# Kernel optimization log

Measured on AMD Instinct MI355X. Metric: run time of the kernel, lower is better.

The kernel has to match this reference:

```python
import jax, jax.numpy as jnp
import numpy as np

B, S, W = 16, 512, 5
H, E, V = 512, 256, 100000


def setup_inputs() -> dict:
    key = jax.random.key(0)
    ks = jax.random.split(key, 20)
    inp = {
        "hiddens": jax.random.normal(ks[0], (B, S, H), jnp.float32),
        "masks": jax.random.randint(ks[1], (B, S), 0, 2, jnp.int32),
        "begins": jax.random.randint(ks[2], (B, S, W), 0, V, jnp.int32),
        "begin_lens": jax.random.randint(ks[3], (B, S), 0, W + 1, jnp.int32),
        "middles": jax.random.randint(ks[4], (B, S, W), 0, V, jnp.int32),
        "middle_lens": jax.random.randint(ks[5], (B, S), 0, W + 1, jnp.int32),
        "ends": jax.random.randint(ks[6], (B, S, W), 0, V, jnp.int32),
        "end_lens": jax.random.randint(ks[7], (B, S), 0, W + 1, jnp.int32),
        # parameters
        "emb": jax.random.normal(ks[8], (V, E), jnp.float32) * 0.02,
        "W_hidden": jax.random.normal(ks[9], (H, 3 * H), jnp.float32) * (1.0 / np.sqrt(H)),
        "b_hidden": jnp.zeros((3 * H,), jnp.float32),
        "W_begin": jax.random.normal(ks[10], (E, 2 * H), jnp.float32) * (1.0 / np.sqrt(E)),
        "b_begin": jnp.zeros((2 * H,), jnp.float32),
        "W_middle": jax.random.normal(ks[11], (E, 2 * H), jnp.float32) * (1.0 / np.sqrt(E)),
        "b_middle": jnp.zeros((2 * H,), jnp.float32),
        "W_end": jax.random.normal(ks[12], (E, 2 * H), jnp.float32) * (1.0 / np.sqrt(E)),
        "b_end": jnp.zeros((2 * H,), jnp.float32),
        "W_gate": jax.random.normal(ks[13], (H, 9), jnp.float32) * (1.0 / np.sqrt(H)),
        "b_gate": jnp.zeros((9,), jnp.float32),
    }
    return inp


def _len_mask(lens, w):
    # True where the lattice candidate is valid (mimics _make_mask's 1s)
    return jnp.arange(w)[None, None, :] < lens[:, :, None]


def _gates(hiddens, masks, W_gate, b_gate):
    b, s, _ = hiddens.shape
    lmr = hiddens @ W_gate + b_gate                      # (B,S,9)
    left, mid, right = jnp.split(lmr, 3, axis=-1)        # each (B,S,3)
    g = jax.nn.sigmoid(left[:, :-2] + mid[:, 1:-1] + right[:, 2:])  # (B,S-2,3)
    ones = jnp.ones((b, 1), g.dtype)
    zeros = jnp.zeros((b, 1), g.dtype)
    begin_g = jnp.concatenate([ones, g[..., 0], ones], axis=1)
    mid_g = jnp.concatenate([zeros, g[..., 1], zeros], axis=1)
    end_g = jnp.concatenate([ones, g[..., 2], ones], axis=1)
    pad = masks == 0
    z = jnp.zeros((), g.dtype)
    return (jnp.where(pad, z, begin_g), jnp.where(pad, z, mid_g), jnp.where(pad, z, end_g))


def reference(hiddens, masks, begins, begin_lens, middles, middle_lens, ends, end_lens,
              emb, W_hidden, b_hidden, W_begin, b_begin, W_middle, b_middle,
              W_end, b_end, W_gate, b_gate):
    w = begins.shape[-1]
    begin_m = _len_mask(begin_lens, w)
    middle_m = _len_mask(middle_lens, w)
    end_m = _len_mask(end_lens, w)

    begin_kv = emb[begins] @ W_begin + b_begin           # (B,S,W,2H)
    middle_kv = emb[middles] @ W_middle + b_middle
    end_kv = emb[ends] @ W_end + b_end

    query, hidden_key, hidden_value = jnp.split(hiddens @ W_hidden + b_hidden, 3, axis=-1)
    bg, mg, eg = _gates(hiddens, masks, W_gate, b_gate)
    begin_kv = bg[:, :, None, None] * begin_kv
    middle_kv = mg[:, :, None, None] * middle_kv
    end_kv = eg[:, :, None, None] * end_kv

    kv = jnp.concatenate([begin_kv, middle_kv, end_kv], axis=-2)   # (B,S,3W,2H)
    h = hiddens.shape[-1]
    keys, values = jnp.split(kv, 2, axis=-1)
    keys = jnp.concatenate([hidden_key[:, :, None, :], keys], axis=-2)     # (B,S,1+3W,H)
    values = jnp.concatenate([hidden_value[:, :, None, :], values], axis=-2)

    # combined mask: True entries get -1e10 (faithful to masked_fill_(masks, -1e10))
    score_mask = jnp.concatenate(
        [(masks != 0)[:, :, None], begin_m, middle_m, end_m], axis=-1)     # (B,S,1+3W)

    scores = jnp.einsum("bsh,bskh->bsk", query, keys)
    scores = jnp.where(score_mask, jnp.asarray(-1e10, scores.dtype), scores)
    weights = jax.nn.softmax(scores, axis=-1)
    return jnp.einsum("bsk,bskh->bsh", weights, values)
```

## Files before the change

kernel.cpp:

```cpp
#include <hip/hip_runtime.h>
#include <cstdint>
#include <cstddef>


typedef unsigned short u16;
typedef _Float16 f16;
typedef __attribute__((ext_vector_type(8))) f16 f16x8;
typedef __attribute__((ext_vector_type(4))) float f32x4;

#define MROWS 8192
#define SS 512

static __device__ __forceinline__ u16 f2h(float x) {
  f16 h = (f16)x;
  return __builtin_bit_cast(u16, h);
}
static __device__ __forceinline__ float h2f(u16 h) {
  return (float)__builtin_bit_cast(f16, h);
}
static __device__ __forceinline__ float sigm(float x) { return 1.f / (1.f + __expf(-x)); }

static __device__ __forceinline__ void gl2lds(const u16* g, u16* l) {
  __builtin_amdgcn_global_load_lds(
      (const __attribute__((address_space(1))) unsigned int*)g,
      (__attribute__((address_space(3))) unsigned int*)l, 16, 0, 0);
}

__global__ __launch_bounds__(256) void prep_xlmr(
    const float* __restrict__ X, const float* __restrict__ Wg,
    const float* __restrict__ bg, u16* __restrict__ Xh,
    float* __restrict__ lmr, float* __restrict__ s0) {
  __shared__ float wg[4608];
  const int t = threadIdx.x;
  if (blockIdx.x < 32) s0[blockIdx.x * 256 + t] = 0.f;
  for (int i = t; i < 4608; i += 256) wg[i] = Wg[i];
  __syncthreads();
  const int lane = t & 63, wid = t >> 6;
#pragma unroll
  for (int it = 0; it < 4; it++) {
    int pos = blockIdx.x * 16 + it * 4 + wid;
    const float* x = X + (size_t)pos * 512 + lane * 8;
    float4 x0 = *(const float4*)x;
    float4 x1 = *(const float4*)(x + 4);
    float xs[8] = {x0.x, x0.y, x0.z, x0.w, x1.x, x1.y, x1.z, x1.w};
    ushort4 h0, h1;
    h0.x = f2h(xs[0]); h0.y = f2h(xs[1]); h0.z = f2h(xs[2]); h0.w = f2h(xs[3]);
    h1.x = f2h(xs[4]); h1.y = f2h(xs[5]); h1.z = f2h(xs[6]); h1.w = f2h(xs[7]);
    ((ushort4*)Xh)[pos * 128 + lane * 2] = h0;
    ((ushort4*)Xh)[pos * 128 + lane * 2 + 1] = h1;
    float p[9];
#pragma unroll
    for (int c = 0; c < 9; c++) p[c] = 0.f;
    const float* wrow = wg + (lane * 8) * 9;
#pragma unroll
    for (int j = 0; j < 8; j++)
#pragma unroll
      for (int c = 0; c < 9; c++) p[c] += xs[j] * wrow[j * 9 + c];
#pragma unroll
    for (int c = 0; c < 9; c++)
#pragma unroll
      for (int o = 32; o > 0; o >>= 1) p[c] += __shfl_xor(p[c], o);
    if (lane == 0) {
#pragma unroll
      for (int c = 0; c < 9; c++) lmr[(size_t)pos * 9 + c] = p[c] + bg[c];
    }
  }
}

__global__ __launch_bounds__(256) void prep_weights(
    const float* __restrict__ Wh, const float* __restrict__ Wb,
    const float* __restrict__ Wm, const float* __restrict__ We,
    const float* __restrict__ bb, const float* __restrict__ bm,
    const float* __restrict__ be, const float* __restrict__ bh,
    const float* __restrict__ lmr, const int* __restrict__ masks,
    u16* __restrict__ Breg, u16* __restrict__ Acat, u16* __restrict__ Whq,
    u16* __restrict__ WvT, float* __restrict__ gates, float* __restrict__ bcat,
    float* __restrict__ u, float* __restrict__ cbuf) {
  __shared__ float tile[64][65];
  const int b = blockIdx.x;
  const int t = threadIdx.x;
  if (b < 64) {
    int k0 = (b & 7) * 64;
    int n0 = (b >> 3) * 64;
#pragma unroll
    for (int i = 0; i < 16; i++) {
      int li = i * 256 + t; int r = li >> 6, c = li & 63;
      tile[r][c] = Wh[(size_t)(k0 + r) * 1536 + 1024 + n0 + c];
    }
    __syncthreads();
#pragma unroll
    for (int i = 0; i < 16; i++) {
      int li = i * 256 + t; int r = li >> 6, c = li & 63;
      Breg[(size_t)(512 + n0 + r) * 512 + k0 + c] = f2h(tile[c][r]);
    }
  } else if (b < 128) {
#pragma unroll
    for (int i = 0; i < 4; i++) {
      int q4 = (b - 64) * 1024 + t * 4 + i;
      int k = q4 >> 7;
      int c4 = (q4 & 127) * 4;
      float4 vq = *(const float4*)(Wh + (size_t)k * 1536 + c4);
      float4 vk = *(const float4*)(Wh + (size_t)k * 1536 + 512 + c4);
      ushort4 qh, kh;
      qh.x = f2h(vq.x); qh.y = f2h(vq.y); qh.z = f2h(vq.z); qh.w = f2h(vq.w);
      kh.x = f2h(vk.x); kh.y = f2h(vk.y); kh.z = f2h(vk.z); kh.w = f2h(vk.w);
      size_t o = (size_t)k * 512 + c4;
      *(ushort4*)(Whq + o) = qh;
      *(ushort4*)(Acat + o) = kh;
    }
  } else if (b < 576) {
    int tid = (b - 128) * 256 + t;
    int n = tid >> 7;
    int kq = (tid & 127) * 4;
    float4 v;
    if (n < 768) {
      int ty = n >> 8, c = n & 255;
      const float* src = (ty == 0 ? Wb : ty == 1 ? Wm : We) + (size_t)c * 1024 + kq;
      v = *(const float4*)src;
    } else if (n < 771) {
      int ty = n - 768;
      const float* src = (ty == 0 ? bb : ty == 1 ? bm : be) + kq;
      v = *(const float4*)src;
    } else {
      v = make_float4(0.f, 0.f, 0.f, 0.f);
    }
    ushort4 h; h.x = f2h(v.x); h.y = f2h(v.y); h.z = f2h(v.z); h.w = f2h(v.w);
    ((ushort4*)(Acat + (size_t)512 * 512))[tid] = h;
  } else if (b < 672) {
    int idx = b - 576;
    int ty = idx >> 5;
    int rem = idx & 31;
    int c0 = (rem & 3) * 64;
    int n0 = (rem >> 2) * 64;
    const float* Wsrc = ty == 0 ? Wb : ty == 1 ? Wm : We;
#pragma unroll
    for (int i = 0; i < 16; i++) {
      int li = i * 256 + t; int r = li >> 6, c = li & 63;
      tile[r][c] = Wsrc[(size_t)(c0 + r) * 1024 + 512 + n0 + c];
    }
    __syncthreads();
#pragma unroll
    for (int i = 0; i < 16; i++) {
      int li = i * 256 + t; int r = li >> 6, c = li & 63;
      WvT[(size_t)(n0 + r) * 768 + ty * 256 + c0 + c] = f2h(tile[c][r]);
    }
  } else if (b < 704) {
    int pos = (b - 672) * 256 + t;
    int s = pos & (SS - 1);
    float g0, g1, g2;
    if (masks[pos] == 0) {
      g0 = g1 = g2 = 0.f;
    } else if (s == 0 || s == SS - 1) {
      g0 = 1.f; g1 = 0.f; g2 = 1.f;
    } else {
      const float* p0 = lmr + (size_t)(pos - 1) * 9;
      const float* p1 = lmr + (size_t)pos * 9;
      const float* p2 = lmr + (size_t)(pos + 1) * 9;
      g0 = sigm(p0[0] + p1[3] + p2[6]);
      g1 = sigm(p0[1] + p1[4] + p2[7]);
      g2 = sigm(p0[2] + p1[5] + p2[8]);
    }
    gates[(size_t)pos * 3 + 0] = g0;
    gates[(size_t)pos * 3 + 1] = g1;
    gates[(size_t)pos * 3 + 2] = g2;
  } else {
    const int lane = t & 63;
    const int widx = (b - 704) * 4 + (t >> 6);
    const int c = lane * 8;
    if (widx < 896) {
      int n = widx;
      float acc = 0.f;
      if (n < 768) {
        int ty = n >> 8, ce = n & 255;
        const float* src = (ty == 0 ? Wb : ty == 1 ? Wm : We) + (size_t)ce * 1024 + c;
        float4 a0 = *(const float4*)src;
        float4 a1 = *(const float4*)(src + 4);
        float4 b0 = *(const float4*)(bh + c);
        float4 b1 = *(const float4*)(bh + c + 4);
        acc = a0.x * b0.x + a0.y * b0.y + a0.z * b0.z + a0.w * b0.w +
              a1.x * b1.x + a1.y * b1.y + a1.z * b1.z + a1.w * b1.w;
      } else if (n < 771) {
        int ty = n - 768;
        const float* src = (ty == 0 ? bb : ty == 1 ? bm : be) + c;
        float4 a0 = *(const float4*)src;
        float4 a1 = *(const float4*)(src + 4);
        float4 b0 = *(const float4*)(bh + c);
        float4 b1 = *(const float4*)(bh + c + 4);
        acc = a0.x * b0.x + a0.y * b0.y + a0.z * b0.z + a0.w * b0.w +
              a1.x * b1.x + a1.y * b1.y + a1.z * b1.z + a1.w * b1.w;
      }
#pragma unroll
      for (int o = 32; o > 0; o >>= 1) acc += __shfl_xor(acc, o);
      if (lane == 0) bcat[512 + n] = acc;
    } else if (widx < 1408) {
      int k = widx - 896;
      const float* wr = Wh + (size_t)k * 1536;
      float4 a0 = *(const float4*)(wr + c);
      float4 a1 = *(const float4*)(wr + c + 4);
      float4 a2 = *(const float4*)(wr + 512 + c);
      float4 a3 = *(const float4*)(wr + 512 + c + 4);
      float4 b0 = *(const float4*)(bh + 512 + c);
      float4 b1 = *(const float4*)(bh + 512 + c + 4);
      float4 b2 = *(const float4*)(bh + c);
      float4 b3 = *(const float4*)(bh + c + 4);
      float acc = a0.x * b0.x + a0.y * b0.y + a0.z * b0.z + a0.w * b0.w +
                  a1.x * b1.x + a1.y * b1.y + a1.z * b1.z + a1.w * b1.w +
                  a2.x * b2.x + a2.y * b2.y + a2.z * b2.z + a2.w * b2.w +
                  a3.x * b3.x + a3.y * b3.y + a3.z * b3.z + a3.w * b3.w;
#pragma unroll
      for (int o = 32; o > 0; o >>= 1) acc += __shfl_xor(acc, o);
      if (lane == 0) u[k] = acc;
    } else if (widx == 1408) {
      float4 b0 = *(const float4*)(bh + c);
      float4 b1 = *(const float4*)(bh + c + 4);
      float4 b2 = *(const float4*)(bh + 512 + c);
      float4 b3 = *(const float4*)(bh + 512 + c + 4);
      float acc = b0.x * b2.x + b0.y * b2.y + b0.z * b2.z + b0.w * b2.w +
                  b1.x * b3.x + b1.y * b3.y + b1.z * b3.z + b1.w * b3.w;
#pragma unroll
      for (int o = 32; o > 0; o >>= 1) acc += __shfl_xor(acc, o);
      if (lane == 0) cbuf[0] = acc;
    } else if (widx < 1417) {
      int i = (widx - 1409) * 64 + lane;
      bcat[i] = bh[1024 + i];
    }
  }
}

template <int MODE>
__global__ __launch_bounds__(256) void gemm_k(
    const u16* __restrict__ A, const u16* __restrict__ Bt,
    const float* __restrict__ ubias, const float* __restrict__ bcat,
    float* __restrict__ Cf, u16* __restrict__ Cb, int Kdim,
    const float* __restrict__ Xf, float* __restrict__ s0) {
  __shared__ __align__(16) u16 As[128 * 32];
  __shared__ __align__(16) u16 Bs[128 * 32];

  const int t = threadIdx.x;
  const int lane = t & 63;
  const int wid = t >> 6;
  const int m0 = blockIdx.x * 128;
  const int n0 = blockIdx.y * 128;
  const int wm = (wid & 1) * 64;
  const int wn = (wid >> 1) * 64;
  const int fr = lane & 15;
  const int kq = (lane >> 4) * 8;

  f32x4 acc[4][4];
#pragma unroll
  for (int i = 0; i < 4; i++)
#pragma unroll
    for (int j = 0; j < 4; j++) acc[i][j] = (f32x4){0.f, 0.f, 0.f, 0.f};

  for (int k0 = 0; k0 < Kdim; k0 += 32) {
    __syncthreads();
#pragma unroll
    for (int p = 0; p < 2; p++) {
      int li = p * 256 + t;
      int row = li >> 2;
      int so = (li & 3) * 8;
      gl2lds(&A[(size_t)(m0 + row) * Kdim + k0 + so], &As[li * 8]);
      gl2lds(&Bt[(size_t)(n0 + row) * Kdim + k0 + so], &Bs[li * 8]);
    }
    __syncthreads();
    f16x8 av[4], bv[4];
#pragma unroll
    for (int i = 0; i < 4; i++) {
      av[i] = *(const f16x8*)&As[(wm + i * 16 + fr) * 32 + kq];
      bv[i] = *(const f16x8*)&Bs[(wn + i * 16 + fr) * 32 + kq];
    }
#pragma unroll
    for (int mt = 0; mt < 4; mt++)
#pragma unroll
      for (int nt = 0; nt < 4; nt++)
        acc[mt][nt] = __builtin_amdgcn_mfma_f32_16x16x32_f16(
            av[mt], bv[nt], acc[mt][nt], 0, 0, 0);
  }

  const int r0 = (lane >> 4) * 4;
  if constexpr (MODE == 0) {
    if (blockIdx.y < 4) {
      float pl[4][4];
#pragma unroll
      for (int mt = 0; mt < 4; mt++)
#pragma unroll
        for (int r = 0; r < 4; r++) pl[mt][r] = 0.f;
#pragma unroll
      for (int mt = 0; mt < 4; mt++)
#pragma unroll
        for (int nt = 0; nt < 4; nt++) {
          int col = n0 + wn + nt * 16 + fr;
          float bv2 = ubias[col];
#pragma unroll
          for (int r = 0; r < 4; r++) {
            int row = m0 + wm + mt * 16 + r0 + r;
            pl[mt][r] += (acc[mt][nt][r] + bv2) * Xf[(size_t)row * 512 + col];
          }
        }
#pragma unroll
      for (int mt = 0; mt < 4; mt++)
#pragma unroll
        for (int r = 0; r < 4; r++) {
          float p = pl[mt][r];
          p += __shfl_xor(p, 1);
          p += __shfl_xor(p, 2);
          p += __shfl_xor(p, 4);
          p += __shfl_xor(p, 8);
          if (fr == r) {
            int row = m0 + wm + mt * 16 + r0 + r;
            atomicAdd(&s0[row], p);
          }
        }
      return;
    }
#pragma unroll
    for (int mt = 0; mt < 4; mt++)
#pragma unroll
      for (int nt = 0; nt < 4; nt++) {
        int col = n0 - 512 + wn + nt * 16 + fr;
        float bv2 = bcat[col];
#pragma unroll
        for (int r = 0; r < 4; r++) {
          int row = m0 + wm + mt * 16 + r0 + r;
          float v = acc[mt][nt][r] + bv2;
          if (col < 512) Cf[(size_t)row * 512 + col] = v;
          else Cb[(size_t)row * 896 + (col - 512)] = f2h(v);
        }
      }
  } else if constexpr (MODE == 1) {
#pragma unroll
    for (int mt = 0; mt < 4; mt++)
#pragma unroll
      for (int nt = 0; nt < 4; nt++) {
        int col = n0 + wn + nt * 16 + fr;
#pragma unroll
        for (int r = 0; r < 4; r++) {
          int row = m0 + wm + mt * 16 + r0 + r;
          int orow = row < 512 ? row : row + 512;
          Cb[(size_t)orow * 512 + col] = f2h(acc[mt][nt][r]);
        }
      }
  } else {
#pragma unroll
    for (int mt = 0; mt < 4; mt++)
#pragma unroll
      for (int nt = 0; nt < 4; nt++) {
        int col = n0 + wn + nt * 16 + fr;
#pragma unroll
        for (int r = 0; r < 4; r++) {
          int row = m0 + wm + mt * 16 + r0 + r;
          Cf[(size_t)row * 512 + col] += acc[mt][nt][r];
        }
      }
  }
}

__global__ __launch_bounds__(256) void attn_kernel(
    const int* __restrict__ masks, const int* __restrict__ begins,
    const int* __restrict__ blens, const int* __restrict__ middles,
    const int* __restrict__ mlens, const int* __restrict__ ends,
    const int* __restrict__ elens, const float* __restrict__ emb,
    const float* __restrict__ HV, const u16* __restrict__ Pb,
    const float* __restrict__ gates, const float* __restrict__ b_begin,
    const float* __restrict__ b_middle, const float* __restrict__ b_end,
    const float* __restrict__ s0buf, const float* __restrict__ cbuf,
    float* __restrict__ out, u16* __restrict__ Ebar) {
  __shared__ float bvs[3][512];
  {
    int tt = threadIdx.x;
    for (int i = tt; i < 512; i += 256) {
      bvs[0][i] = b_begin[512 + i];
      bvs[1][i] = b_middle[512 + i];
      bvs[2][i] = b_end[512 + i];
    }
  }
  __syncthreads();
  const int t = threadIdx.x;
  const int lane = t & 63;
  const int wid = t >> 6;
  const int pos = blockIdx.x * 4 + wid;
  const int mask = masks[pos];
  const float* hvp = HV + (size_t)pos * 512;
  float4 hv0 = *(const float4*)(hvp + lane * 8);
  float4 hv1 = *(const float4*)(hvp + lane * 8 + 4);
  float* orow = out + (size_t)pos * 512;
  u16* erow = Ebar + (size_t)pos * 768;

  if (mask == 0) {
    float s0 = s0buf[pos] + cbuf[0];
    int nv = min(blens[pos], 5) + min(mlens[pos], 5) + min(elens[pos], 5);
    int ninv = 15 - nv;
    float w0;
    if (ninv == 0) {
      w0 = 1.f;
    } else {
      float Mx = fmaxf(s0, 0.f);
      float e0 = __expf(s0 - Mx);
      w0 = e0 / (e0 + (float)ninv * __expf(-Mx));
    }
    float4 o0, o1;
    o0.x = w0 * hv0.x; o0.y = w0 * hv0.y; o0.z = w0 * hv0.z; o0.w = w0 * hv0.w;
    o1.x = w0 * hv1.x; o1.y = w0 * hv1.y; o1.z = w0 * hv1.z; o1.w = w0 * hv1.w;
    *(float4*)(orow + lane * 8) = o0;
    *(float4*)(orow + lane * 8 + 4) = o1;
    ushort4 zz; zz.x = zz.y = zz.z = zz.w = 0;
    *(ushort4*)(erow + 0 * 256 + lane * 4) = zz;
    *(ushort4*)(erow + 1 * 256 + lane * 4) = zz;
    *(ushort4*)(erow + 2 * 256 + lane * 4) = zz;
  } else {
    float g[3];
    g[0] = gates[(size_t)pos * 3 + 0];
    g[1] = gates[(size_t)pos * 3 + 1];
    g[2] = gates[(size_t)pos * 3 + 2];
    const u16* prow = Pb + (size_t)pos * 896;
    float4 Pt[3];
    float qb[3];
#pragma unroll
    for (int ty = 0; ty < 3; ty++) {
      ushort4 pu = *(const ushort4*)(prow + ty * 256 + lane * 4);
      Pt[ty].x = h2f(pu.x); Pt[ty].y = h2f(pu.y);
      Pt[ty].z = h2f(pu.z); Pt[ty].w = h2f(pu.w);
      qb[ty] = h2f(prow[768 + ty]);
    }
    int lens[3] = {blens[pos], mlens[pos], elens[pos]};
    const int* ib = begins + (size_t)pos * 5;
    const int* im = middles + (size_t)pos * 5;
    const int* ie = ends + (size_t)pos * 5;
    float4 ev[3][5];
#pragma unroll
    for (int w = 0; w < 5; w++) {
      ev[0][w] = *(const float4*)(emb + (size_t)ib[w] * 256 + lane * 4);
      ev[1][w] = *(const float4*)(emb + (size_t)im[w] * 256 + lane * 4);
      ev[2][w] = *(const float4*)(emb + (size_t)ie[w] * 256 + lane * 4);
    }
    float sc[16];
    sc[0] = -1e10f;
#pragma unroll
    for (int ty = 0; ty < 3; ty++) {
#pragma unroll
      for (int w = 0; w < 5; w++) {
        float4 e = ev[ty][w];
        float d = Pt[ty].x * e.x + Pt[ty].y * e.y + Pt[ty].z * e.z + Pt[ty].w * e.w;
#pragma unroll
        for (int o = 32; o > 0; o >>= 1) d += __shfl_xor(d, o);
        sc[1 + ty * 5 + w] = (w < lens[ty]) ? -1e10f : g[ty] * (d + qb[ty]);
      }
    }
    float Mx = sc[0];
#pragma unroll
    for (int k = 1; k < 16; k++) Mx = fmaxf(Mx, sc[k]);
    float wts[16];
    float zs = 0.f;
#pragma unroll
    for (int k = 0; k < 16; k++) {
      wts[k] = __expf(sc[k] - Mx);
      zs += wts[k];
    }
    float inv = 1.f / zs;
    float alpha[3];
#pragma unroll
    for (int ty = 0; ty < 3; ty++) {
      float ax = 0.f, ay = 0.f, az = 0.f, aw = 0.f, asum = 0.f;
#pragma unroll
      for (int w = 0; w < 5; w++) {
        float wk = wts[1 + ty * 5 + w];
        asum += wk;
        ax += wk * ev[ty][w].x;
        ay += wk * ev[ty][w].y;
        az += wk * ev[ty][w].z;
        aw += wk * ev[ty][w].w;
      }
      float sg = g[ty] * inv;
      alpha[ty] = sg * asum;
      ushort4 h;
      h.x = f2h(ax * sg); h.y = f2h(ay * sg); h.z = f2h(az * sg); h.w = f2h(aw * sg);
      *(ushort4*)(erow + ty * 256 + lane * 4) = h;
    }
    float w0 = wts[0] * inv;
    float4 o0, o1;
    int hb = lane * 8;
    o0.x = w0 * hv0.x + alpha[0] * bvs[0][hb + 0] + alpha[1] * bvs[1][hb + 0] + alpha[2] * bvs[2][hb + 0];
    o0.y = w0 * hv0.y + alpha[0] * bvs[0][hb + 1] + alpha[1] * bvs[1][hb + 1] + alpha[2] * bvs[2][hb + 1];
    o0.z = w0 * hv0.z + alpha[0] * bvs[0][hb + 2] + alpha[1] * bvs[1][hb + 2] + alpha[2] * bvs[2][hb + 2];
    o0.w = w0 * hv0.w + alpha[0] * bvs[0][hb + 3] + alpha[1] * bvs[1][hb + 3] + alpha[2] * bvs[2][hb + 3];
    o1.x = w0 * hv1.x + alpha[0] * bvs[0][hb + 4] + alpha[1] * bvs[1][hb + 4] + alpha[2] * bvs[2][hb + 4];
    o1.y = w0 * hv1.y + alpha[0] * bvs[0][hb + 5] + alpha[1] * bvs[1][hb + 5] + alpha[2] * bvs[2][hb + 5];
    o1.z = w0 * hv1.z + alpha[0] * bvs[0][hb + 6] + alpha[1] * bvs[1][hb + 6] + alpha[2] * bvs[2][hb + 6];
    o1.w = w0 * hv1.w + alpha[0] * bvs[0][hb + 7] + alpha[1] * bvs[1][hb + 7] + alpha[2] * bvs[2][hb + 7];
    *(float4*)(orow + lane * 8) = o0;
    *(float4*)(orow + lane * 8 + 4) = o1;
  }
}

extern "C" void kernel_launch(void* const* d_in, const int* in_sizes, int n_in,
                              void* d_out, int out_size, void* d_ws, size_t ws_size,
                              hipStream_t stream) {
  const float* hiddens = (const float*)d_in[0];
  const int* masks = (const int*)d_in[1];
  const int* begins = (const int*)d_in[2];
  const int* blens = (const int*)d_in[3];
  const int* middles = (const int*)d_in[4];
  const int* mlens = (const int*)d_in[5];
  const int* ends = (const int*)d_in[6];
  const int* elens = (const int*)d_in[7];
  const float* emb = (const float*)d_in[8];
  const float* Wh = (const float*)d_in[9];
  const float* bh = (const float*)d_in[10];
  const float* Wb = (const float*)d_in[11];
  const float* bb = (const float*)d_in[12];
  const float* Wm = (const float*)d_in[13];
  const float* bm = (const float*)d_in[14];
  const float* We = (const float*)d_in[15];
  const float* be = (const float*)d_in[16];
  const float* Wg = (const float*)d_in[17];
  const float* bg = (const float*)d_in[18];
  float* out = (float*)d_out;

  char* ws = (char*)d_ws;
  size_t off = 0;
  auto alloc = [&](size_t bytes) -> char* {
    char* p = ws + off;
    off += (bytes + 255) & ~(size_t)255;
    return p;
  };
  u16* Xh = (u16*)alloc((size_t)8192 * 512 * 2);
  u16* Whq = (u16*)alloc((size_t)512 * 512 * 2);
  u16* Acat = (u16*)alloc((size_t)1408 * 512 * 2);
  u16* Breg = (u16*)alloc((size_t)1920 * 512 * 2);
  u16* WvT = (u16*)alloc((size_t)512 * 768 * 2);
  float* HV = (float*)alloc((size_t)8192 * 512 * 4);
  u16* Pb = (u16*)alloc((size_t)8192 * 896 * 2);
  float* lmr = (float*)alloc((size_t)8192 * 9 * 4);
  float* gates = (float*)alloc((size_t)8192 * 3 * 4);
  float* s0 = (float*)alloc((size_t)8192 * 4);
  float* bcat = (float*)alloc((size_t)1408 * 4);
  float* u = (float*)alloc((size_t)512 * 4);
  float* cbuf = (float*)alloc((size_t)4);
  u16* Ebar = (u16*)alloc((size_t)8192 * 768 * 2);
  if (off > ws_size) return;

  prep_xlmr<<<512, 256, 0, stream>>>(hiddens, Wg, bg, Xh, lmr, s0);
  prep_weights<<<1059, 256, 0, stream>>>(Wh, Wb, Wm, We, bb, bm, be, bh, lmr,
                                         masks, Breg, Acat, Whq, WvT, gates,
                                         bcat, u, cbuf);
  gemm_k<1><<<dim3(11, 4), 256, 0, stream>>>(
      Acat, Whq, nullptr, nullptr, nullptr, Breg, 512, nullptr, nullptr);
  gemm_k<0><<<dim3(64, 15), 256, 0, stream>>>(
      Xh, Breg, u, bcat, HV, Pb, 512, hiddens, s0);
  attn_kernel<<<2048, 256, 0, stream>>>(masks, begins, blens, middles, mlens, ends,
                                        elens, emb, HV, Pb, gates, bb, bm, be,
                                        s0, cbuf, out, Ebar);
  gemm_k<2><<<dim3(64, 4), 256, 0, stream>>>(
      Ebar, WvT, nullptr, nullptr, out, nullptr, 768, nullptr, nullptr);
}
```

Measured before the change: 290.2 us.

## Merge prep kernels, store hidden values in fp16, fold output combine into final GEMM

```diff
diff --git a/kernel.cpp b/kernel.cpp
--- a/kernel.cpp
+++ b/kernel.cpp
@@ -26,57 +26,18 @@
       (__attribute__((address_space(3))) unsigned int*)l, 16, 0, 0);
 }
 
-__global__ __launch_bounds__(256) void prep_xlmr(
+__global__ __launch_bounds__(256) void prep_all(
     const float* __restrict__ X, const float* __restrict__ Wg,
-    const float* __restrict__ bg, u16* __restrict__ Xh,
-    float* __restrict__ lmr, float* __restrict__ s0) {
-  __shared__ float wg[4608];
-  const int t = threadIdx.x;
-  if (blockIdx.x < 32) s0[blockIdx.x * 256 + t] = 0.f;
-  for (int i = t; i < 4608; i += 256) wg[i] = Wg[i];
-  __syncthreads();
-  const int lane = t & 63, wid = t >> 6;
-#pragma unroll
-  for (int it = 0; it < 4; it++) {
-    int pos = blockIdx.x * 16 + it * 4 + wid;
-    const float* x = X + (size_t)pos * 512 + lane * 8;
-    float4 x0 = *(const float4*)x;
-    float4 x1 = *(const float4*)(x + 4);
-    float xs[8] = {x0.x, x0.y, x0.z, x0.w, x1.x, x1.y, x1.z, x1.w};
-    ushort4 h0, h1;
-    h0.x = f2h(xs[0]); h0.y = f2h(xs[1]); h0.z = f2h(xs[2]); h0.w = f2h(xs[3]);
-    h1.x = f2h(xs[4]); h1.y = f2h(xs[5]); h1.z = f2h(xs[6]); h1.w = f2h(xs[7]);
-    ((ushort4*)Xh)[pos * 128 + lane * 2] = h0;
-    ((ushort4*)Xh)[pos * 128 + lane * 2 + 1] = h1;
-    float p[9];
-#pragma unroll
-    for (int c = 0; c < 9; c++) p[c] = 0.f;
-    const float* wrow = wg + (lane * 8) * 9;
-#pragma unroll
-    for (int j = 0; j < 8; j++)
-#pragma unroll
-      for (int c = 0; c < 9; c++) p[c] += xs[j] * wrow[j * 9 + c];
-#pragma unroll
-    for (int c = 0; c < 9; c++)
-#pragma unroll
-      for (int o = 32; o > 0; o >>= 1) p[c] += __shfl_xor(p[c], o);
-    if (lane == 0) {
-#pragma unroll
-      for (int c = 0; c < 9; c++) lmr[(size_t)pos * 9 + c] = p[c] + bg[c];
-    }
-  }
-}
-
-__global__ __launch_bounds__(256) void prep_weights(
-    const float* __restrict__ Wh, const float* __restrict__ Wb,
-    const float* __restrict__ Wm, const float* __restrict__ We,
-    const float* __restrict__ bb, const float* __restrict__ bm,
-    const float* __restrict__ be, const float* __restrict__ bh,
-    const float* __restrict__ lmr, const int* __restrict__ masks,
-    u16* __restrict__ Breg, u16* __restrict__ Acat, u16* __restrict__ Whq,
-    u16* __restrict__ WvT, float* __restrict__ gates, float* __restrict__ bcat,
-    float* __restrict__ u, float* __restrict__ cbuf) {
-  __shared__ float tile[64][65];
+    const float* __restrict__ bg, const float* __restrict__ Wh,
+    const float* __restrict__ Wb, const float* __restrict__ Wm,
+    const float* __restrict__ We, const float* __restrict__ bb,
+    const float* __restrict__ bm, const float* __restrict__ be,
+    const float* __restrict__ bh, u16* __restrict__ Xh,
+    float* __restrict__ lmr, float* __restrict__ s0, u16* __restrict__ Breg,
+    u16* __restrict__ Acat, u16* __restrict__ Whq, u16* __restrict__ WvT,
+    float* __restrict__ bcat, float* __restrict__ u, float* __restrict__ cbuf) {
+  __shared__ float shmem[4608];
+#define TI(r, c) shmem[(r)*65 + (c)]
   const int b = blockIdx.x;
   const int t = threadIdx.x;
   if (b < 64) {
@@ -85,13 +46,13 @@
 #pragma unroll
     for (int i = 0; i < 16; i++) {
       int li = i * 256 + t; int r = li >> 6, c = li & 63;
-      tile[r][c] = Wh[(size_t)(k0 + r) * 1536 + 1024 + n0 + c];
+      TI(r, c) = Wh[(size_t)(k0 + r) * 1536 + 1024 + n0 + c];
     }
     __syncthreads();
 #pragma unroll
     for (int i = 0; i < 16; i++) {
       int li = i * 256 + t; int r = li >> 6, c = li & 63;
-      Breg[(size_t)(512 + n0 + r) * 512 + k0 + c] = f2h(tile[c][r]);
+      Breg[(size_t)(512 + n0 + r) * 512 + k0 + c] = f2h(TI(c, r));
     }
   } else if (b < 128) {
 #pragma unroll
@@ -136,52 +97,30 @@
 #pragma unroll
     for (int i = 0; i < 16; i++) {
       int li = i * 256 + t; int r = li >> 6, c = li & 63;
-      tile[r][c] = Wsrc[(size_t)(c0 + r) * 1024 + 512 + n0 + c];
+      TI(r, c) = Wsrc[(size_t)(c0 + r) * 1024 + 512 + n0 + c];
     }
     __syncthreads();
 #pragma unroll
     for (int i = 0; i < 16; i++) {
       int li = i * 256 + t; int r = li >> 6, c = li & 63;
-      WvT[(size_t)(n0 + r) * 768 + ty * 256 + c0 + c] = f2h(tile[c][r]);
-    }
-  } else if (b < 704) {
-    int pos = (b - 672) * 256 + t;
-    int s = pos & (SS - 1);
-    float g0, g1, g2;
-    if (masks[pos] == 0) {
-      g0 = g1 = g2 = 0.f;
-    } else if (s == 0 || s == SS - 1) {
-      g0 = 1.f; g1 = 0.f; g2 = 1.f;
-    } else {
-      const float* p0 = lmr + (size_t)(pos - 1) * 9;
-      const float* p1 = lmr + (size_t)pos * 9;
-      const float* p2 = lmr + (size_t)(pos + 1) * 9;
-      g0 = sigm(p0[0] + p1[3] + p2[6]);
-      g1 = sigm(p0[1] + p1[4] + p2[7]);
-      g2 = sigm(p0[2] + p1[5] + p2[8]);
-    }
-    gates[(size_t)pos * 3 + 0] = g0;
-    gates[(size_t)pos * 3 + 1] = g1;
-    gates[(size_t)pos * 3 + 2] = g2;
-  } else {
+      WvT[(size_t)(n0 + r) * 768 + ty * 256 + c0 + c] = f2h(TI(c, r));
+    }
+  } else if (b < 1028) {
     const int lane = t & 63;
-    const int widx = (b - 704) * 4 + (t >> 6);
+    const int widx = (b - 672) * 4 + (t >> 6);
     const int c = lane * 8;
     if (widx < 896) {
       int n = widx;
       float acc = 0.f;
-      if (n < 768) {
-        int ty = n >> 8, ce = n & 255;
-        const float* src = (ty == 0 ? Wb : ty == 1 ? Wm : We) + (size_t)ce * 1024 + c;
-        float4 a0 = *(const float4*)src;
-        float4 a1 = *(const float4*)(src + 4);
-        float4 b0 = *(const float4*)(bh + c);
-        float4 b1 = *(const float4*)(bh + c + 4);
-        acc = a0.x * b0.x + a0.y * b0.y + a0.z * b0.z + a0.w * b0.w +
-              a1.x * b1.x + a1.y * b1.y + a1.z * b1.z + a1.w * b1.w;
-      } else if (n < 771) {
-        int ty = n - 768;
-        const float* src = (ty == 0 ? bb : ty == 1 ? bm : be) + c;
+      if (n < 771) {
+        const float* src;
+        if (n < 768) {
+          int ty = n >> 8, ce = n & 255;
+          src = (ty == 0 ? Wb : ty == 1 ? Wm : We) + (size_t)ce * 1024 + c;
+        } else {
+          int ty = n - 768;
+          src = (ty == 0 ? bb : ty == 1 ? bm : be) + c;
+        }
         float4 a0 = *(const float4*)src;
         float4 a1 = *(const float4*)(src + 4);
         float4 b0 = *(const float4*)(bh + c);
@@ -224,7 +163,43 @@
       int i = (widx - 1409) * 64 + lane;
       bcat[i] = bh[1024 + i];
     }
+  } else {
+    const int xb = b - 1028;
+    if (xb < 32) s0[xb * 256 + t] = 0.f;
+    for (int i = t; i < 4608; i += 256) shmem[i] = Wg[i];
+    __syncthreads();
+    const int lane = t & 63, wid = t >> 6;
+#pragma unroll
+    for (int it = 0; it < 4; it++) {
+      int pos = xb * 16 + it * 4 + wid;
+      const float* x = X + (size_t)pos * 512 + lane * 8;
+      float4 x0 = *(const float4*)x;
+      float4 x1 = *(const float4*)(x + 4);
+      float xs[8] = {x0.x, x0.y, x0.z, x0.w, x1.x, x1.y, x1.z, x1.w};
+      ushort4 h0, h1;
+      h0.x = f2h(xs[0]); h0.y = f2h(xs[1]); h0.z = f2h(xs[2]); h0.w = f2h(xs[3]);
+      h1.x = f2h(xs[4]); h1.y = f2h(xs[5]); h1.z = f2h(xs[6]); h1.w = f2h(xs[7]);
+      ((ushort4*)Xh)[pos * 128 + lane * 2] = h0;
+      ((ushort4*)Xh)[pos * 128 + lane * 2 + 1] = h1;
+      float p[9];
+#pragma unroll
+      for (int c = 0; c < 9; c++) p[c] = 0.f;
+      const float* wrow = shmem + (lane * 8) * 9;
+#pragma unroll
+      for (int j = 0; j < 8; j++)
+#pragma unroll
+        for (int c = 0; c < 9; c++) p[c] += xs[j] * wrow[j * 9 + c];
+#pragma unroll
+      for (int c = 0; c < 9; c++)
+#pragma unroll
+        for (int o = 32; o > 0; o >>= 1) p[c] += __shfl_xor(p[c], o);
+      if (lane == 0) {
+#pragma unroll
+        for (int c = 0; c < 9; c++) lmr[(size_t)pos * 9 + c] = p[c] + bg[c];
+      }
+    }
   }
+#undef TI
 }
 
 template <int MODE>
@@ -232,7 +207,10 @@
     const u16* __restrict__ A, const u16* __restrict__ Bt,
     const float* __restrict__ ubias, const float* __restrict__ bcat,
     float* __restrict__ Cf, u16* __restrict__ Cb, int Kdim,
-    const float* __restrict__ Xf, float* __restrict__ s0) {
+    const u16* __restrict__ Xh, float* __restrict__ s0,
+    const float4* __restrict__ sc4, const u16* __restrict__ HPb,
+    const float* __restrict__ bb, const float* __restrict__ bm,
+    const float* __restrict__ be) {
   __shared__ __align__(16) u16 As[128 * 32];
   __shared__ __align__(16) u16 Bs[128 * 32];
 
@@ -294,7 +272,7 @@
 #pragma unroll
           for (int r = 0; r < 4; r++) {
             int row = m0 + wm + mt * 16 + r0 + r;
-            pl[mt][r] += (acc[mt][nt][r] + bv2) * Xf[(size_t)row * 512 + col];
+            pl[mt][r] += (acc[mt][nt][r] + bv2) * h2f(Xh[(size_t)row * 512 + col]);
           }
         }
 #pragma unroll
@@ -322,9 +300,7 @@
 #pragma unroll
         for (int r = 0; r < 4; r++) {
           int row = m0 + wm + mt * 16 + r0 + r;
-          float v = acc[mt][nt][r] + bv2;
-          if (col < 512) Cf[(size_t)row * 512 + col] = v;
-          else Cb[(size_t)row * 896 + (col - 512)] = f2h(v);
+          Cb[(size_t)row * 1408 + col] = f2h(acc[mt][nt][r] + bv2);
         }
       }
   } else if constexpr (MODE == 1) {
@@ -346,10 +322,16 @@
 #pragma unroll
       for (int nt = 0; nt < 4; nt++) {
         int col = n0 + wn + nt * 16 + fr;
+        float b0 = bb[512 + col];
+        float b1 = bm[512 + col];
+        float b2 = be[512 + col];
 #pragma unroll
         for (int r = 0; r < 4; r++) {
           int row = m0 + wm + mt * 16 + r0 + r;
-          Cf[(size_t)row * 512 + col] += acc[mt][nt][r];
+          float4 s = sc4[row];
+          float hv = h2f(HPb[(size_t)row * 1408 + col]);
+          Cf[(size_t)row * 512 + col] =
+              s.x * hv + s.y * b0 + s.z * b1 + s.w * b2 + acc[mt][nt][r];
         }
       }
   }
@@ -360,35 +342,21 @@
     const int* __restrict__ blens, const int* __restrict__ middles,
     const int* __restrict__ mlens, const int* __restrict__ ends,
     const int* __restrict__ elens, const float* __restrict__ emb,
-    const float* __restrict__ HV, const u16* __restrict__ Pb,
-    const float* __restrict__ gates, const float* __restrict__ b_begin,
-    const float* __restrict__ b_middle, const float* __restrict__ b_end,
+    const u16* __restrict__ HPb, const float* __restrict__ lmr,
     const float* __restrict__ s0buf, const float* __restrict__ cbuf,
-    float* __restrict__ out, u16* __restrict__ Ebar) {
-  __shared__ float bvs[3][512];
-  {
-    int tt = threadIdx.x;
-    for (int i = tt; i < 512; i += 256) {
-      bvs[0][i] = b_begin[512 + i];
-      bvs[1][i] = b_middle[512 + i];
-      bvs[2][i] = b_end[512 + i];
-    }
-  }
-  __syncthreads();
+    float4* __restrict__ sc4, u16* __restrict__ Ebar) {
   const int t = threadIdx.x;
   const int lane = t & 63;
   const int wid = t >> 6;
   const int pos = blockIdx.x * 4 + wid;
   const int mask = masks[pos];
-  const float* hvp = HV + (size_t)pos * 512;
-  float4 hv0 = *(const float4*)(hvp + lane * 8);
-  float4 hv1 = *(const float4*)(hvp + lane * 8 + 4);
-  float* orow = out + (size_t)pos * 512;
   u16* erow = Ebar + (size_t)pos * 768;
+
+  int l0 = min(blens[pos], 5), l1 = min(mlens[pos], 5), l2 = min(elens[pos], 5);
+  int nv = l0 + l1 + l2;
 
   if (mask == 0) {
     float s0 = s0buf[pos] + cbuf[0];
-    int nv = min(blens[pos], 5) + min(mlens[pos], 5) + min(elens[pos], 5);
     int ninv = 15 - nv;
     float w0;
     if (ninv == 0) {
@@ -398,64 +366,80 @@
       float e0 = __expf(s0 - Mx);
       w0 = e0 / (e0 + (float)ninv * __expf(-Mx));
     }
-    float4 o0, o1;
-    o0.x = w0 * hv0.x; o0.y = w0 * hv0.y; o0.z = w0 * hv0.z; o0.w = w0 * hv0.w;
-    o1.x = w0 * hv1.x; o1.y = w0 * hv1.y; o1.z = w0 * hv1.z; o1.w = w0 * hv1.w;
-    *(float4*)(orow + lane * 8) = o0;
-    *(float4*)(orow + lane * 8 + 4) = o1;
+    if (lane == 0) sc4[pos] = make_float4(w0, 0.f, 0.f, 0.f);
     ushort4 zz; zz.x = zz.y = zz.z = zz.w = 0;
     *(ushort4*)(erow + 0 * 256 + lane * 4) = zz;
     *(ushort4*)(erow + 1 * 256 + lane * 4) = zz;
     *(ushort4*)(erow + 2 * 256 + lane * 4) = zz;
   } else {
+    const int s = pos & (SS - 1);
     float g[3];
-    g[0] = gates[(size_t)pos * 3 + 0];
-    g[1] = gates[(size_t)pos * 3 + 1];
-    g[2] = gates[(size_t)pos * 3 + 2];
-    const u16* prow = Pb + (size_t)pos * 896;
+    if (s == 0 || s == SS - 1) {
+      g[0] = 1.f; g[1] = 0.f; g[2] = 1.f;
+    } else {
+      const float* p0 = lmr + (size_t)(pos - 1) * 9;
+      const float* p1 = lmr + (size_t)pos * 9;
+      const float* p2 = lmr + (size_t)(pos + 1) * 9;
+      g[0] = sigm(p0[0] + p1[3] + p2[6]);
+      g[1] = sigm(p0[1] + p1[4] + p2[7]);
+      g[2] = sigm(p0[2] + p1[5] + p2[8]);
+    }
+    const bool deg = (nv == 15);
+    int l[3] = {l0, l1, l2};
+    if (deg) { l[0] = 0; l[1] = 0; l[2] = 0; }
+
     float4 Pt[3];
     float qb[3];
+    if (!deg) {
+      const u16* prow = HPb + (size_t)pos * 1408 + 512;
+#pragma unroll
+      for (int ty = 0; ty < 3; ty++) {
+        ushort4 pu = *(const ushort4*)(prow + ty * 256 + lane * 4);
+        Pt[ty].x = h2f(pu.x); Pt[ty].y = h2f(pu.y);
+        Pt[ty].z = h2f(pu.z); Pt[ty].w = h2f(pu.w);
+        qb[ty] = h2f(prow[768 + ty]);
+      }
+    }
+    const int* idxp[3];
+    idxp[0] = begins + (size_t)pos * 5;
+    idxp[1] = middles + (size_t)pos * 5;
+    idxp[2] = ends + (size_t)pos * 5;
+
+    float4 ev[3][5];
+    float scv[3][5];
+    float Mx = deg ? 0.f : -3.0e38f;
 #pragma unroll
     for (int ty = 0; ty < 3; ty++) {
-      ushort4 pu = *(const ushort4*)(prow + ty * 256 + lane * 4);
-      Pt[ty].x = h2f(pu.x); Pt[ty].y = h2f(pu.y);
-      Pt[ty].z = h2f(pu.z); Pt[ty].w = h2f(pu.w);
-      qb[ty] = h2f(prow[768 + ty]);
-    }
-    int lens[3] = {blens[pos], mlens[pos], elens[pos]};
-    const int* ib = begins + (size_t)pos * 5;
-    const int* im = middles + (size_t)pos * 5;
-    const int* ie = ends + (size_t)pos * 5;
-    float4 ev[3][5];
-#pragma unroll
-    for (int w = 0; w < 5; w++) {
-      ev[0][w] = *(const float4*)(emb + (size_t)ib[w] * 256 + lane * 4);
-      ev[1][w] = *(const float4*)(emb + (size_t)im[w] * 256 + lane * 4);
-      ev[2][w] = *(const float4*)(emb + (size_t)ie[w] * 256 + lane * 4);
-    }
-    float sc[16];
-    sc[0] = -1e10f;
-#pragma unroll
-    for (int ty = 0; ty < 3; ty++) {
 #pragma unroll
       for (int w = 0; w < 5; w++) {
-        float4 e = ev[ty][w];
-        float d = Pt[ty].x * e.x + Pt[ty].y * e.y + Pt[ty].z * e.z + Pt[ty].w * e.w;
-#pragma unroll
-        for (int o = 32; o > 0; o >>= 1) d += __shfl_xor(d, o);
-        sc[1 + ty * 5 + w] = (w < lens[ty]) ? -1e10f : g[ty] * (d + qb[ty]);
-      }
-    }
-    float Mx = sc[0];
-#pragma unroll
-    for (int k = 1; k < 16; k++) Mx = fmaxf(Mx, sc[k]);
-    float wts[16];
-    float zs = 0.f;
-#pragma unroll
-    for (int k = 0; k < 16; k++) {
-      wts[k] = __expf(sc[k] - Mx);
-      zs += wts[k];
-    }
+        bool act = (w >= l[ty]);
+        if (act) {
+          ev[ty][w] = *(const float4*)(emb + (size_t)idxp[ty][w] * 256 + lane * 4);
+          float sv = 0.f;
+          if (!deg) {
+            float4 e = ev[ty][w];
+            float d = Pt[ty].x * e.x + Pt[ty].y * e.y + Pt[ty].z * e.z + Pt[ty].w * e.w;
+#pragma unroll
+            for (int o = 32; o > 0; o >>= 1) d += __shfl_xor(d, o);
+            sv = g[ty] * (d + qb[ty]);
+          }
+          scv[ty][w] = sv;
+          Mx = fmaxf(Mx, sv);
+        }
+      }
+    }
+    float wts0 = deg ? 1.f : 0.f;
+    float zs = wts0;
+    float wts[3][5];
+#pragma unroll
+    for (int ty = 0; ty < 3; ty++)
+#pragma unroll
+      for (int w = 0; w < 5; w++) {
+        bool act = (w >= l[ty]);
+        float wv = act ? __expf(scv[ty][w] - Mx) : 0.f;
+        wts[ty][w] = wv;
+        zs += wv;
+      }
     float inv = 1.f / zs;
     float alpha[3];
 #pragma unroll
@@ -463,12 +447,14 @@
       float ax = 0.f, ay = 0.f, az = 0.f, aw = 0.f, asum = 0.f;
 #pragma unroll
       for (int w = 0; w < 5; w++) {
-        float wk = wts[1 + ty * 5 + w];
-        asum += wk;
-        ax += wk * ev[ty][w].x;
-        ay += wk * ev[ty][w].y;
-        az += wk * ev[ty][w].z;
-        aw += wk * ev[ty][w].w;
+        if (w >= l[ty]) {
+          float wk = wts[ty][w];
+          asum += wk;
+          ax += wk * ev[ty][w].x;
+          ay += wk * ev[ty][w].y;
+          az += wk * ev[ty][w].z;
+          aw += wk * ev[ty][w].w;
+        }
       }
       float sg = g[ty] * inv;
       alpha[ty] = sg * asum;
@@ -476,19 +462,7 @@
       h.x = f2h(ax * sg); h.y = f2h(ay * sg); h.z = f2h(az * sg); h.w = f2h(aw * sg);
       *(ushort4*)(erow + ty * 256 + lane * 4) = h;
     }
-    float w0 = wts[0] * inv;
-    float4 o0, o1;
-    int hb = lane * 8;
-    o0.x = w0 * hv0.x + alpha[0] * bvs[0][hb + 0] + alpha[1] * bvs[1][hb + 0] + alpha[2] * bvs[2][hb + 0];
-    o0.y = w0 * hv0.y + alpha[0] * bvs[0][hb + 1] + alpha[1] * bvs[1][hb + 1] + alpha[2] * bvs[2][hb + 1];
-    o0.z = w0 * hv0.z + alpha[0] * bvs[0][hb + 2] + alpha[1] * bvs[1][hb + 2] + alpha[2] * bvs[2][hb + 2];
-    o0.w = w0 * hv0.w + alpha[0] * bvs[0][hb + 3] + alpha[1] * bvs[1][hb + 3] + alpha[2] * bvs[2][hb + 3];
-    o1.x = w0 * hv1.x + alpha[0] * bvs[0][hb + 4] + alpha[1] * bvs[1][hb + 4] + alpha[2] * bvs[2][hb + 4];
-    o1.y = w0 * hv1.y + alpha[0] * bvs[0][hb + 5] + alpha[1] * bvs[1][hb + 5] + alpha[2] * bvs[2][hb + 5];
-    o1.z = w0 * hv1.z + alpha[0] * bvs[0][hb + 6] + alpha[1] * bvs[1][hb + 6] + alpha[2] * bvs[2][hb + 6];
-    o1.w = w0 * hv1.w + alpha[0] * bvs[0][hb + 7] + alpha[1] * bvs[1][hb + 7] + alpha[2] * bvs[2][hb + 7];
-    *(float4*)(orow + lane * 8) = o0;
-    *(float4*)(orow + lane * 8 + 4) = o1;
+    if (lane == 0) sc4[pos] = make_float4(wts0 * inv, alpha[0], alpha[1], alpha[2]);
   }
 }
 
@@ -528,28 +502,29 @@
   u16* Acat = (u16*)alloc((size_t)1408 * 512 * 2);
   u16* Breg = (u16*)alloc((size_t)1920 * 512 * 2);
   u16* WvT = (u16*)alloc((size_t)512 * 768 * 2);
-  float* HV = (float*)alloc((size_t)8192 * 512 * 4);
-  u16* Pb = (u16*)alloc((size_t)8192 * 896 * 2);
+  u16* HPb = (u16*)alloc((size_t)8192 * 1408 * 2);
   float* lmr = (float*)alloc((size_t)8192 * 9 * 4);
-  float* gates = (float*)alloc((size_t)8192 * 3 * 4);
   float* s0 = (float*)alloc((size_t)8192 * 4);
   float* bcat = (float*)alloc((size_t)1408 * 4);
   float* u = (float*)alloc((size_t)512 * 4);
   float* cbuf = (float*)alloc((size_t)4);
+  float* sc4 = (float*)alloc((size_t)8192 * 4 * 4);
   u16* Ebar = (u16*)alloc((size_t)8192 * 768 * 2);
   if (off > ws_size) return;
 
-  prep_xlmr<<<512, 256, 0, stream>>>(hiddens, Wg, bg, Xh, lmr, s0);
-  prep_weights<<<1059, 256, 0, stream>>>(Wh, Wb, Wm, We, bb, bm, be, bh, lmr,
-                                         masks, Breg, Acat, Whq, WvT, gates,
-                                         bcat, u, cbuf);
+  prep_all<<<1540, 256, 0, stream>>>(hiddens, Wg, bg, Wh, Wb, Wm, We, bb, bm, be,
+                                     bh, Xh, lmr, s0, Breg, Acat, Whq, WvT,
+                                     bcat, u, cbuf);
   gemm_k<1><<<dim3(11, 4), 256, 0, stream>>>(
-      Acat, Whq, nullptr, nullptr, nullptr, Breg, 512, nullptr, nullptr);
+      Acat, Whq, nullptr, nullptr, nullptr, Breg, 512, nullptr, nullptr,
+      nullptr, nullptr, nullptr, nullptr, nullptr);
   gemm_k<0><<<dim3(64, 15), 256, 0, stream>>>(
-      Xh, Breg, u, bcat, HV, Pb, 512, hiddens, s0);
-  attn_kernel<<<2048, 256, 0, stream>>>(masks, begins, blens, middles, mlens, ends,
-                                        elens, emb, HV, Pb, gates, bb, bm, be,
-                                        s0, cbuf, out, Ebar);
+      Xh, Breg, u, bcat, nullptr, HPb, 512, Xh, s0,
+      nullptr, nullptr, nullptr, nullptr, nullptr);
+  attn_kernel<<<2048, 256, 0, stream>>>(masks, begins, blens, middles, mlens,
+                                        ends, elens, emb, HPb, lmr, s0, cbuf,
+                                        (float4*)sc4, Ebar);
   gemm_k<2><<<dim3(64, 4), 256, 0, stream>>>(
-      Ebar, WvT, nullptr, nullptr, out, nullptr, 768, nullptr, nullptr);
-}
+      Ebar, WvT, nullptr, nullptr, out, nullptr, 768, nullptr, nullptr,
+      (const float4*)sc4, HPb, bb, bm, be);
+}
```

Measured after the change: 288.0 us. About the same (-0.8%).
